# Optimization experiments

Measured on AMD Instinct MI355X. Metric: run time of the kernel, lower is better.

The kernel has to match this reference:

```python
import jax, jax.numpy as jnp
import numpy as np

K = 20
EPS = 1e-6


def _vnt_linear(x, W):
    # VNT linear: rows normalized to sum to 1 (translation-equivariant channel mix)
    Wn = W / W.sum(axis=1, keepdims=True)
    return jnp.einsum('oi,bi...->bo...', Wn, x)


def _vn_lrelu(p, d):
    # Vector-neuron LeakyReLU with negative_slope=0: project p off -d half-space
    dot = jnp.sum(p * d, axis=2, keepdims=True)   # axis 2 is the 3-vector axis
    dns = jnp.sum(d * d, axis=2, keepdims=True)
    return jnp.where(dot >= 0, p, p - (dot / (dns + EPS)) * d)


def _vnt_lin_lrelu(x, W, D):
    p = _vnt_linear(x, W)
    d = jnp.einsum('oi,bi...->bo...', D, x)
    return _vn_lrelu(p, d)


def _graph_feature_cross(pts, k):
    # pts: [B, N, 3] -> edge features [B, 3(ch), 3(vec), N, k]
    B = pts.shape[0]
    xx = jnp.sum(pts * pts, axis=-1)                       # [B, N]
    inner = jnp.einsum('bnd,bmd->bnm', pts, pts)           # [B, N, N]
    pairwise = 2.0 * inner - xx[:, :, None] - xx[:, None, :]  # -||xi-xj||^2
    _, idx = jax.lax.top_k(pairwise, k)                    # [B, N, k]
    b_idx = jnp.arange(B)[:, None, None]
    nbrs = pts[b_idx, idx]                                 # [B, N, k, 3]
    ctr = jnp.broadcast_to(pts[:, :, None, :], nbrs.shape)
    cross = jnp.cross(nbrs, ctr)
    feat = jnp.stack([nbrs - ctr, ctr, cross], axis=3)     # [B, N, k, 3ch, 3vec]
    return jnp.transpose(feat, (0, 3, 4, 1, 2))            # [B, 3, 3, N, k]


def setup_inputs() -> dict:
    key = jax.random.key(0)
    ks = jax.random.split(key, 9)
    B, N, hidden = 8, 2048, 128

    def w(k_, o, i):  # positive weights -> stable row-sum normalization
        return jax.random.uniform(k_, (o, i), jnp.float32, 0.5 / i, 1.5 / i)

    def d(k_, o, i):
        return jax.random.normal(k_, (o, i), jnp.float32) / np.sqrt(i)

    return {
        'pc': jax.random.normal(ks[0], (B, N, 3), jnp.float32),
        'W_pos': w(ks[1], 64, 3), 'D_pos': d(ks[2], 64, 3),
        'W1': w(ks[3], hidden, 64), 'D1': d(ks[4], hidden, 64),
        'W2': w(ks[5], hidden, 2 * hidden), 'D2': d(ks[6], hidden, 2 * hidden),
        'W3': w(ks[7], hidden, 2 * hidden), 'D3': d(ks[8], hidden, 2 * hidden),
    }


def reference(pc, W_pos, D_pos, W1, D1, W2, D2, W3, D3):
    feat = _graph_feature_cross(pc, K)               # [B, 3, 3, N, k]
    net = _vnt_lin_lrelu(feat, W_pos, D_pos)         # [B, 64, 3, N, k]
    net = net.mean(axis=-1)                          # pool over k -> [B, 64, 3, N]
    net = _vnt_lin_lrelu(net, W1, D1)                # [B, 128, 3, N]
    pooled = jnp.broadcast_to(net.mean(axis=-1, keepdims=True), net.shape)
    net = jnp.concatenate([net, pooled], axis=1)     # [B, 256, 3, N]
    net = _vnt_lin_lrelu(net, W2, D2)                # [B, 128, 3, N]
    pooled = jnp.broadcast_to(net.mean(axis=-1, keepdims=True), net.shape)
    net = jnp.concatenate([net, pooled], axis=1)     # [B, 256, 3, N]
    net = _vnt_lin_lrelu(net, W3, D3)                # [B, 128, 3, N]
    c = net.mean(axis=-1)                            # pool over N -> [B, 128, 3]
    return c.reshape(pc.shape[0], -1)                # [B, 384]
```

## Files before the change

### kernel.cpp

```cpp
#include <hip/hip_runtime.h>
#include <hip/hip_bf16.h>
#include <math.h>

constexpr int B = 8;
constexpr int N = 2048;
constexpr int KNN = 20;
constexpr int H = 128;
constexpr int P = 3 * N;
constexpr int QPW = 8;

constexpr int OSB2   = 0;
constexpr int OWT2   = 8448;
constexpr int OWT3   = 41216;
constexpr int OPS1   = 73984;
constexpr int OPS2   = 98560;
constexpr int OOUTS  = 123136;
constexpr int OBAR   = 147712;
constexpr int OSB3   = 148736;
constexpr int OWB1   = 160000;
constexpr int OWB2   = 176384;
constexpr int OWB3   = 209152;
constexpr int OXP0   = 569600;

constexpr int ZERO_BASE = OPS1;
constexpr int ZERO_CNT  = 74752;

constexpr int GRID_VNT  = 1024;
constexpr int BLK_PER_B = 128;

typedef __attribute__((ext_vector_type(8))) short bf16x8;
typedef __attribute__((ext_vector_type(4))) float f32x4;

__device__ __forceinline__ unsigned short f2bf(float x) {
  __hip_bfloat16 h = __float2bfloat16(x);
  return *(unsigned short*)&h;
}
__device__ __forceinline__ float bf2f(unsigned short u) {
  __hip_bfloat16 h;
  *(unsigned short*)&h = u;
  return __bfloat162float(h);
}
__device__ __forceinline__ unsigned int packhl(float x) {
  unsigned short hi = f2bf(x);
  float lo = x - bf2f(hi);
  unsigned short ls = f2bf(lo);
  return (unsigned)hi | ((unsigned)ls << 16);
}

__device__ __forceinline__ float cohload(const float* p) {
  return __hip_atomic_load(p, __ATOMIC_RELAXED, __HIP_MEMORY_SCOPE_AGENT);
}
__device__ __forceinline__ void cohstore(float* p, float v) {
  __hip_atomic_store(p, v, __ATOMIC_RELAXED, __HIP_MEMORY_SCOPE_AGENT);
}

__device__ __forceinline__ void wave_sort_key(unsigned long long& k, int lane) {
#pragma unroll
  for (int kk = 2; kk <= 64; kk <<= 1) {
#pragma unroll
    for (int j = kk >> 1; j > 0; j >>= 1) {
      unsigned long long pk =
          (unsigned long long)__shfl_xor((long long)k, j);
      bool iam_lower   = (lane & j) == 0;
      bool dir_desc    = (lane & kk) == 0;
      bool p_better    = pk > k;
      bool want_better = (dir_desc == iam_lower);
      k = (p_better == want_better) ? pk : k;
    }
  }
}

__global__ __launch_bounds__(512, 8) void knn_edge_kernel(
    const float* __restrict__ pc, const float* __restrict__ Wpos,
    const float* __restrict__ Dp,
    const float* __restrict__ W1, const float* __restrict__ D1,
    const float* __restrict__ W2, const float* __restrict__ D2,
    const float* __restrict__ W3, const float* __restrict__ D3,
    float* __restrict__ ws) {
  __shared__ float4 spt[N];
  __shared__ __align__(16) unsigned char sphase[QPW][640];
  int tid = threadIdx.x;
  int b = blockIdx.y;
  int bid = blockIdx.y * gridDim.x + blockIdx.x;
  int wv = tid >> 6, lane = tid & 63;
  unsigned short* Xp0 = (unsigned short*)(ws + OXP0);
  unsigned short* sbufw = (unsigned short*)sphase[wv];
  float4* erw = (float4*)sphase[wv];

  int o = lane;
  float w0 = Wpos[o * 3 + 0], w1 = Wpos[o * 3 + 1], w2 = Wpos[o * 3 + 2];
  float e0 = Dp[o * 3 + 0], e1 = Dp[o * 3 + 1], e2 = Dp[o * 3 + 2];

  {
    int zi = bid * 512 + tid;
    if (zi < ZERO_CNT) ws[ZERO_BASE + zi] = 0.f;
  }
  if (bid < 96) {
    int rr = bid * 8 + wv;
    const float* src;
    float* tdst = nullptr;
    unsigned int* pdst;
    int C, Cpack;
    bool norm;
    if (rr < 128)      { src = W1 + rr * 64;            C = 64;  Cpack = 64;  norm = true;
                         pdst = (unsigned int*)(ws + OWB1) + rr * 16; }
    else if (rr < 256) { int m = rr - 128; src = D1 + m * 64;  C = 64;  Cpack = 64;  norm = false;
                         pdst = (unsigned int*)(ws + OWB1) + (m + 128) * 16; }
    else if (rr < 384) { int m = rr - 256; src = W2 + m * 256; C = 256; Cpack = 128; norm = true;
                         pdst = (unsigned int*)(ws + OWB2) + m * 16; tdst = ws + OWT2 + m; }
    else if (rr < 512) { int m = rr - 384; src = D2 + m * 256; C = 256; Cpack = 128; norm = false;
                         pdst = (unsigned int*)(ws + OWB2) + (m + 128) * 16; tdst = ws + OWT2 + 128 + m; }
    else if (rr < 640) { int m = rr - 512; src = W3 + m * 256; C = 256; Cpack = 128; norm = true;
                         pdst = (unsigned int*)(ws + OWB3) + m * 16; tdst = ws + OWT3 + m; }
    else               { int m = rr - 640; src = D3 + m * 256; C = 256; Cpack = 128; norm = false;
                         pdst = (unsigned int*)(ws + OWB3) + (m + 128) * 16; tdst = ws + OWT3 + 128 + m; }
    float s = 1.f;
    if (norm) {
      float a = 0.f;
      for (int i = lane; i < C; i += 64) a += src[i];
#pragma unroll
      for (int off = 32; off > 0; off >>= 1) a += __shfl_xor(a, off);
      s = a;
    }
    for (int i = lane; i < C; i += 64) {
      float val = src[i] / s;
      if (i < Cpack) pdst[(i >> 4) * 4096 + (i & 15)] = packhl(val);
      if (tdst && i >= 128) tdst[(i - 128) * 256] = val;
    }
  }

  const float* pcb = pc + (size_t)b * N * 3;
  for (int i = tid; i < N; i += 512) {
    float x = pcb[i * 3 + 0], y = pcb[i * 3 + 1], z = pcb[i * 3 + 2];
    float xx = __fadd_rn(__fadd_rn(__fmul_rn(x, x), __fmul_rn(y, y)), __fmul_rn(z, z));
    spt[i] = make_float4(2.f * x, 2.f * y, 2.f * z, xx);
  }
  __syncthreads();
  int q = blockIdx.x * QPW + wv;
  float4 qp = spt[q];
  float qx = 0.5f * qp.x, qy = 0.5f * qp.y, qz = 0.5f * qp.z, qxx = qp.w;

  float dv[32];
  float lmax = -INFINITY;
#pragma unroll
  for (int i = 0; i < 32; ++i) {
    float4 m = spt[i * 64 + lane];
    float A = __fadd_rn(__fadd_rn(__fmul_rn(m.x, qx), __fmul_rn(m.y, qy)),
                        __fmul_rn(m.z, qz));
    float d = __fsub_rn(__fsub_rn(A, qxx), m.w);
    dv[i] = d;
    lmax = fmaxf(lmax, d);
  }

  float sv = lmax;
#pragma unroll
  for (int k = 2; k <= 64; k <<= 1) {
#pragma unroll
    for (int j = k >> 1; j > 0; j >>= 1) {
      float pv = __shfl_xor(sv, j);
      bool keep_max = ((lane & k) == 0) == ((lane & j) == 0);
      sv = keep_max ? fmaxf(sv, pv) : fminf(sv, pv);
    }
  }
  float tval = __shfl(sv, 19);

  unsigned msk = 0u;
#pragma unroll
  for (int i = 0; i < 32; ++i) msk |= (dv[i] >= tval) ? (1u << i) : 0u;
  int cnt = __popc(msk);
  int scan = cnt;
#pragma unroll
  for (int off = 1; off < 64; off <<= 1) {
    int t = __shfl_up(scan, off);
    scan += (lane >= off) ? t : 0;
  }
  int S = __shfl(scan, 63);
  int pos = scan - cnt;
  unsigned mm = msk;
  while (mm) {
    int i = __ffs(mm) - 1;
    mm &= mm - 1;
    if (pos < 192) sbufw[pos] = (unsigned short)(i * 64 + lane);
    ++pos;
  }

  auto distOf = [&](int m) -> float {
    float4 mp = spt[m];
    float A = __fadd_rn(__fadd_rn(__fmul_rn(mp.x, qx), __fmul_rn(mp.y, qy)),
                        __fmul_rn(mp.z, qz));
    return __fsub_rn(__fsub_rn(A, qxx), mp.w);
  };
  auto mkkey = [&](int m) -> unsigned long long {
    float d = distOf(m);
    unsigned u = __float_as_uint(d);
    u ^= (u >> 31) ? 0xFFFFFFFFu : 0x80000000u;
    return ((unsigned long long)u << 32) | (unsigned)(~m);
  };

  unsigned long long key = 0ULL;
  if (S <= 64) {
    if (lane < S) key = mkkey(sbufw[lane]);
    wave_sort_key(key, lane);
  } else if (S <= 192) {
    int p2 = 0;
    while (p2 < S) {
      if (lane >= KNN) {
        int t = p2 + lane - KNN;
        key = (t < S) ? mkkey(sbufw[t]) : 0ULL;
      }
      wave_sort_key(key, lane);
      p2 += 64 - KNN;
    }
  } else {
    int p2 = 0;
    while (p2 < N) {
      if (lane >= KNN) {
        int t = p2 + lane - KNN;
        key = (t < N) ? mkkey(t) : 0ULL;
      }
      wave_sort_key(key, lane);
      p2 += 64 - KNN;
    }
  }
  int cm = ~((unsigned)key);

  if (lane < KNN) {
    float4 t = spt[cm];
    float nx = 0.5f * t.x, ny = 0.5f * t.y, nz = 0.5f * t.z;
    float ex = nx - qx, ey = ny - qy, ez = nz - qz;
    float rx = ny * qz - nz * qy;
    float ry = nz * qx - nx * qz;
    float rz = nx * qy - ny * qx;
    erw[2 * lane + 0] = make_float4(ex, ey, ez, 0.f);
    erw[2 * lane + 1] = make_float4(rx, ry, rz, 0.f);
  }

  {
    float s = (w0 + w2) + w1;
    w0 = w0 / s; w1 = w1 / s; w2 = w2 / s;
  }
  float cx = qx, cy = qy, cz = qz;
  float pcx = w1 * cx, pcy = w1 * cy, pcz = w1 * cz;
  float dcx = e1 * cx, dcy = e1 * cy, dcz = e1 * cz;
  float ax = 0.f, ay = 0.f, az = 0.f;
#pragma unroll 4
  for (int k = 0; k < KNN; ++k) {
    float4 e4 = erw[2 * k + 0];
    float4 r4 = erw[2 * k + 1];
    float ex = e4.x, ey = e4.y, ez = e4.z;
    float rx = r4.x, ry = r4.y, rz = r4.z;
    float px = fmaf(w0, ex, fmaf(w2, rx, pcx));
    float py = fmaf(w0, ey, fmaf(w2, ry, pcy));
    float pz = fmaf(w0, ez, fmaf(w2, rz, pcz));
    float dx = fmaf(e0, ex, fmaf(e2, rx, dcx));
    float dy = fmaf(e0, ey, fmaf(e2, ry, dcy));
    float dz = fmaf(e0, ez, fmaf(e2, rz, dcz));
    float dot = fmaf(px, dx, fmaf(py, dy, pz * dz));
    float dns = fmaf(dx, dx, fmaf(dy, dy, dz * dz)) + 1e-6f;
    float r0 = __builtin_amdgcn_rcpf(dns);
    r0 = r0 * fmaf(-dns, r0, 2.0f);
    float f = (dot < 0.f) ? dot * r0 : 0.f;
    ax = fmaf(-f, dx, px) + ax;
    ay = fmaf(-f, dy, py) + ay;
    az = fmaf(-f, dz, pz) + az;
  }
  int pbase = ((q >> 4) * 48) + (q & 15);
  unsigned short* dst = Xp0 + ((size_t)b * P + pbase) * 128 + 2 * o;
  *(unsigned int*)(dst)              = packhl(ax * (1.f / 20.f));
  *(unsigned int*)(dst + 16 * 128)   = packhl(ay * (1.f / 20.f));
  *(unsigned int*)(dst + 32 * 128)   = packhl(az * (1.f / 20.f));
}

template <int K2, bool HASPOOL, bool LAST, bool GSRC>
__device__ __forceinline__ void vnt_layer_body(
    unsigned short* xt, float* sb, float* spool,
    const unsigned short* __restrict__ Xp, const unsigned short* __restrict__ Wb,
    const float* __restrict__ ps, const float* __restrict__ Wt,
    float* __restrict__ sbg, unsigned int* sbflag,
    float* __restrict__ pool, float* __restrict__ outs,
    unsigned int* wait_cnt, unsigned int* arrive_cnt,
    int b, int nt, int p0, int tid) {
  constexpr int KS = K2 / 32;
  constexpr int LDR = K2 + 8;
  constexpr int LDO = 132;
  float* ot = (float*)xt;
  int w = tid >> 6, lane = tid & 63;
  int q = lane >> 4, cl = lane & 15;

  if constexpr (GSRC) {
    for (int ch = tid; ch < 48 * (K2 / 8); ch += 256) {
      int rp = ch / (K2 / 8), cc = ch % (K2 / 8);
      *(uint4*)(xt + rp * LDR + cc * 8) =
          *(const uint4*)(Xp + ((size_t)b * P + p0 + rp) * K2 + cc * 8);
    }
  }

  bf16x8 acur[2][2], anxt[2][2];
#pragma unroll
  for (int t = 0; t < 2; ++t)
#pragma unroll
    for (int pd = 0; pd < 2; ++pd)
      acur[t][pd] = *(const bf16x8*)(Wb +
          (size_t)(32 * w + 16 * t + 128 * pd + cl) * 32 + q * 8);

  if constexpr (HASPOOL) {
    if (nt == 0) {
      if (tid == 0) {
        while (__hip_atomic_load(wait_cnt, __ATOMIC_RELAXED,
                                 __HIP_MEMORY_SCOPE_AGENT) < (unsigned)BLK_PER_B) {
          __builtin_amdgcn_s_sleep(2);
        }
      }
      __syncthreads();
      for (int i = tid; i < 384; i += 256) {
        float x = 0.f;
#pragma unroll
        for (int k = 0; k < 8; ++k)
          x += cohload(&ps[k * 3072 + b * 384 + i]);
        spool[i] = x * (1.f / 2048.f);
      }
      __syncthreads();
      float s0 = 0.f, s1 = 0.f, s2 = 0.f;
#pragma unroll 16
      for (int c = 0; c < 128; ++c) {
        float x = Wt[c * 256 + tid];
        s0 = fmaf(x, spool[c * 3 + 0], s0);
        s1 = fmaf(x, spool[c * 3 + 1], s1);
        s2 = fmaf(x, spool[c * 3 + 2], s2);
      }
      sb[tid * 3 + 0] = s0;
      sb[tid * 3 + 1] = s1;
      sb[tid * 3 + 2] = s2;
      cohstore(&sbg[tid * 3 + 0], s0);
      cohstore(&sbg[tid * 3 + 1], s1);
      cohstore(&sbg[tid * 3 + 2], s2);
      __syncthreads();
      if (tid == 0)
        __hip_atomic_fetch_add(sbflag, 1u, __ATOMIC_RELAXED,
                               __HIP_MEMORY_SCOPE_AGENT);
    } else {
      if (tid == 0) {
        while (__hip_atomic_load(sbflag, __ATOMIC_RELAXED,
                                 __HIP_MEMORY_SCOPE_AGENT) < 1u) {
          __builtin_amdgcn_s_sleep(2);
        }
      }
      __syncthreads();
      for (int i = tid; i < 768; i += 256) sb[i] = cohload(&sbg[i]);
      __syncthreads();
    }
  } else {
    __syncthreads();
  }

  f32x4 acc[2][2][3] = {};

#pragma unroll
  for (int ks = 0; ks < KS; ++ks) {
    if (ks + 1 < KS) {
#pragma unroll
      for (int t = 0; t < 2; ++t)
#pragma unroll
        for (int pd = 0; pd < 2; ++pd)
          anxt[t][pd] = *(const bf16x8*)(Wb +
              (size_t)(32 * w + 16 * t + 128 * pd + cl) * 32 + q * 8 +
              (ks + 1) * 8192);
    }
    bf16x8 bb[3];
#pragma unroll
    for (int v = 0; v < 3; ++v)
      bb[v] = *(const bf16x8*)(xt + (v * 16 + cl) * LDR + ks * 32 + q * 8);
#pragma unroll
    for (int t = 0; t < 2; ++t)
#pragma unroll
      for (int pd = 0; pd < 2; ++pd)
#pragma unroll
        for (int v = 0; v < 3; ++v)
          acc[t][pd][v] = __builtin_amdgcn_mfma_f32_16x16x32_bf16(
              acur[t][pd], bb[v], acc[t][pd][v], 0, 0, 0);
#pragma unroll
    for (int t = 0; t < 2; ++t)
#pragma unroll
      for (int pd = 0; pd < 2; ++pd)
        acur[t][pd] = anxt[t][pd];
  }
  __syncthreads();

#pragma unroll
  for (int t = 0; t < 2; ++t) {
    float res[3][4];
#pragma unroll
    for (int r = 0; r < 4; ++r) {
      int o = 32 * w + 16 * t + 4 * q + r;
      float pv[3], dvv[3];
#pragma unroll
      for (int v = 0; v < 3; ++v) {
        pv[v] = acc[t][0][v][r] + (HASPOOL ? sb[o * 3 + v] : 0.f);
        dvv[v] = acc[t][1][v][r] + (HASPOOL ? sb[(128 + o) * 3 + v] : 0.f);
      }
      float dot = fmaf(pv[0], dvv[0], fmaf(pv[1], dvv[1], pv[2] * dvv[2]));
      float dns = fmaf(dvv[0], dvv[0], fmaf(dvv[1], dvv[1], dvv[2] * dvv[2]));
      float f = (dot < 0.f) ? dot / (dns + 1e-6f) : 0.f;
#pragma unroll
      for (int v = 0; v < 3; ++v) res[v][r] = pv[v] - f * dvv[v];
    }
    int o0 = 32 * w + 16 * t + 4 * q;
#pragma unroll
    for (int v = 0; v < 3; ++v) {
      f32x4 rv = {res[v][0], res[v][1], res[v][2], res[v][3]};
      *(f32x4*)(ot + (v * 16 + cl) * LDO + o0) = rv;
    }
  }
  __syncthreads();

  int shadow = (nt & 7) * 3072;
  for (int s = tid; s < 384; s += 256) {
    int o = s / 3, v = s % 3;
    float a2 = 0.f;
#pragma unroll
    for (int c = 0; c < 16; ++c) a2 += ot[(v * 16 + c) * LDO + o];
    if (LAST) atomicAdd(outs + shadow + b * 384 + s, a2);
    else      atomicAdd(pool + shadow + b * 384 + s, a2);
  }

  __syncthreads();
  if (arrive_cnt != nullptr && tid == 0) {
    __hip_atomic_fetch_add(arrive_cnt, 1u, __ATOMIC_RELAXED,
                           __HIP_MEMORY_SCOPE_AGENT);
  }

  if constexpr (!LAST) {
    for (int s = tid; s < 1536; s += 256) {
      int pix = s >> 5, c4 = s & 31;
      float4 sv = *(float4*)(ot + pix * LDO + c4 * 4);
      uint4 vv;
      vv.x = packhl(sv.x);
      vv.y = packhl(sv.y);
      vv.z = packhl(sv.z);
      vv.w = packhl(sv.w);
      *(uint4*)(xt + pix * 264 + c4 * 8) = vv;
    }
  }
}

__global__ __launch_bounds__(256, 4) void vnt_stack_kernel(
    float* __restrict__ ws, float* __restrict__ out) {
  __shared__ __align__(16) char smem[48 * 132 * 4];
  __shared__ float sb[768];
  __shared__ float spool[384];
  __shared__ unsigned int last_flag;
  int tid = threadIdx.x;
  int bid = blockIdx.x;
  int b = bid >> 7;
  int nt = bid & 127;
  int p0 = nt * 48;
  unsigned short* xt = (unsigned short*)smem;
  unsigned int* bar = (unsigned int*)(ws + OBAR);
  unsigned int* cnt1 = bar + b * 32;
  unsigned int* cnt2 = bar + 256 + b * 32;
  unsigned int* cntm = bar + 512;
  unsigned int* sbf2 = bar + 576 + b * 16;
  unsigned int* sbf3 = bar + 704 + b * 16;

  vnt_layer_body<128, false, false, true>(
      xt, sb, spool,
      (const unsigned short*)(ws + OXP0), (const unsigned short*)(ws + OWB1),
      nullptr, nullptr, nullptr, nullptr, ws + OPS1, nullptr,
      nullptr, cnt1, b, nt, p0, tid);

  vnt_layer_body<256, true, false, false>(
      xt, sb, spool,
      nullptr, (const unsigned short*)(ws + OWB2),
      ws + OPS1, ws + OWT2, ws + OSB2 + b * 768, sbf2, ws + OPS2, nullptr,
      cnt1, cnt2, b, nt, p0, tid);

  vnt_layer_body<256, true, true, false>(
      xt, sb, spool,
      nullptr, (const unsigned short*)(ws + OWB3),
      ws + OPS2, ws + OWT3, ws + OSB3 + b * 768, sbf3, nullptr, ws + OOUTS,
      cnt2, nullptr, b, nt, p0, tid);

  if (tid == 0) {
    unsigned old = __hip_atomic_fetch_add(cntm, 1u, __ATOMIC_RELAXED,
                                          __HIP_MEMORY_SCOPE_AGENT);
    last_flag = (old == (unsigned)GRID_VNT - 1) ? 1u : 0u;
  }
  __syncthreads();
  if (last_flag) {
    const float* outs = ws + OOUTS;
    for (int idx = tid; idx < B * 384; idx += 256) {
      float s = 0.f;
#pragma unroll
      for (int k = 0; k < 8; ++k) s += cohload(&outs[k * 3072 + idx]);
      out[idx] = s * (1.f / 2048.f);
    }
  }
}

extern "C" void kernel_launch(void* const* d_in, const int* in_sizes, int n_in,
                              void* d_out, int out_size, void* d_ws, size_t ws_size,
                              hipStream_t stream) {
  (void)in_sizes; (void)n_in; (void)out_size; (void)ws_size;
  const float* pc   = (const float*)d_in[0];
  const float* Wpos = (const float*)d_in[1];
  const float* Dpos = (const float*)d_in[2];
  const float* W1   = (const float*)d_in[3];
  const float* D1   = (const float*)d_in[4];
  const float* W2   = (const float*)d_in[5];
  const float* D2   = (const float*)d_in[6];
  const float* W3   = (const float*)d_in[7];
  const float* D3   = (const float*)d_in[8];
  float* out = (float*)d_out;
  float* ws  = (float*)d_ws;

  knn_edge_kernel<<<dim3(N / QPW, B), 512, 0, stream>>>(
      pc, Wpos, Dpos, W1, D1, W2, D2, W3, D3, ws);

  vnt_stack_kernel<<<GRID_VNT, 256, 0, stream>>>(ws, out);
}
```

Baseline: 164.2 us.

## Fuse kNN edge-feature stage into VNT stack kernel via shared-memory handoff

Result: faster. 157.3 us (median of 2 runs) (-4.2%).

```diff
diff --git a/kernel.cpp b/kernel.cpp
--- a/kernel.cpp
+++ b/kernel.cpp
@@ -7,7 +7,6 @@
 constexpr int KNN = 20;
 constexpr int H = 128;
 constexpr int P = 3 * N;
-constexpr int QPW = 8;
 
 constexpr int OSB2   = 0;
 constexpr int OWT2   = 8448;
@@ -20,10 +19,10 @@
 constexpr int OWB1   = 160000;
 constexpr int OWB2   = 176384;
 constexpr int OWB3   = 209152;
-constexpr int OXP0   = 569600;
 
 constexpr int ZERO_BASE = OPS1;
 constexpr int ZERO_CNT  = 74752;
+constexpr int PREP_BLOCKS = (ZERO_CNT + 255) / 256;
 
 constexpr int GRID_VNT  = 1024;
 constexpr int BLK_PER_B = 128;
@@ -70,211 +69,60 @@
   }
 }
 
-__global__ __launch_bounds__(512, 8) void knn_edge_kernel(
-    const float* __restrict__ pc, const float* __restrict__ Wpos,
-    const float* __restrict__ Dp,
+__global__ __launch_bounds__(256) void prep_kernel(
     const float* __restrict__ W1, const float* __restrict__ D1,
     const float* __restrict__ W2, const float* __restrict__ D2,
     const float* __restrict__ W3, const float* __restrict__ D3,
     float* __restrict__ ws) {
-  __shared__ float4 spt[N];
-  __shared__ __align__(16) unsigned char sphase[QPW][640];
   int tid = threadIdx.x;
-  int b = blockIdx.y;
-  int bid = blockIdx.y * gridDim.x + blockIdx.x;
-  int wv = tid >> 6, lane = tid & 63;
-  unsigned short* Xp0 = (unsigned short*)(ws + OXP0);
-  unsigned short* sbufw = (unsigned short*)sphase[wv];
-  float4* erw = (float4*)sphase[wv];
-
-  int o = lane;
-  float w0 = Wpos[o * 3 + 0], w1 = Wpos[o * 3 + 1], w2 = Wpos[o * 3 + 2];
-  float e0 = Dp[o * 3 + 0], e1 = Dp[o * 3 + 1], e2 = Dp[o * 3 + 2];
-
+  int bid = blockIdx.x;
   {
-    int zi = bid * 512 + tid;
+    int zi = bid * 256 + tid;
     if (zi < ZERO_CNT) ws[ZERO_BASE + zi] = 0.f;
   }
   if (bid < 96) {
-    int rr = bid * 8 + wv;
-    const float* src;
-    float* tdst = nullptr;
-    unsigned int* pdst;
-    int C, Cpack;
-    bool norm;
-    if (rr < 128)      { src = W1 + rr * 64;            C = 64;  Cpack = 64;  norm = true;
-                         pdst = (unsigned int*)(ws + OWB1) + rr * 16; }
-    else if (rr < 256) { int m = rr - 128; src = D1 + m * 64;  C = 64;  Cpack = 64;  norm = false;
-                         pdst = (unsigned int*)(ws + OWB1) + (m + 128) * 16; }
-    else if (rr < 384) { int m = rr - 256; src = W2 + m * 256; C = 256; Cpack = 128; norm = true;
-                         pdst = (unsigned int*)(ws + OWB2) + m * 16; tdst = ws + OWT2 + m; }
-    else if (rr < 512) { int m = rr - 384; src = D2 + m * 256; C = 256; Cpack = 128; norm = false;
-                         pdst = (unsigned int*)(ws + OWB2) + (m + 128) * 16; tdst = ws + OWT2 + 128 + m; }
-    else if (rr < 640) { int m = rr - 512; src = W3 + m * 256; C = 256; Cpack = 128; norm = true;
-                         pdst = (unsigned int*)(ws + OWB3) + m * 16; tdst = ws + OWT3 + m; }
-    else               { int m = rr - 640; src = D3 + m * 256; C = 256; Cpack = 128; norm = false;
-                         pdst = (unsigned int*)(ws + OWB3) + (m + 128) * 16; tdst = ws + OWT3 + 128 + m; }
-    float s = 1.f;
-    if (norm) {
-      float a = 0.f;
-      for (int i = lane; i < C; i += 64) a += src[i];
-#pragma unroll
-      for (int off = 32; off > 0; off >>= 1) a += __shfl_xor(a, off);
-      s = a;
-    }
-    for (int i = lane; i < C; i += 64) {
-      float val = src[i] / s;
-      if (i < Cpack) pdst[(i >> 4) * 4096 + (i & 15)] = packhl(val);
-      if (tdst && i >= 128) tdst[(i - 128) * 256] = val;
-    }
-  }
-
-  const float* pcb = pc + (size_t)b * N * 3;
-  for (int i = tid; i < N; i += 512) {
-    float x = pcb[i * 3 + 0], y = pcb[i * 3 + 1], z = pcb[i * 3 + 2];
-    float xx = __fadd_rn(__fadd_rn(__fmul_rn(x, x), __fmul_rn(y, y)), __fmul_rn(z, z));
-    spt[i] = make_float4(2.f * x, 2.f * y, 2.f * z, xx);
-  }
-  __syncthreads();
-  int q = blockIdx.x * QPW + wv;
-  float4 qp = spt[q];
-  float qx = 0.5f * qp.x, qy = 0.5f * qp.y, qz = 0.5f * qp.z, qxx = qp.w;
-
-  float dv[32];
-  float lmax = -INFINITY;
-#pragma unroll
-  for (int i = 0; i < 32; ++i) {
-    float4 m = spt[i * 64 + lane];
-    float A = __fadd_rn(__fadd_rn(__fmul_rn(m.x, qx), __fmul_rn(m.y, qy)),
-                        __fmul_rn(m.z, qz));
-    float d = __fsub_rn(__fsub_rn(A, qxx), m.w);
-    dv[i] = d;
-    lmax = fmaxf(lmax, d);
-  }
-
-  float sv = lmax;
-#pragma unroll
-  for (int k = 2; k <= 64; k <<= 1) {
-#pragma unroll
-    for (int j = k >> 1; j > 0; j >>= 1) {
-      float pv = __shfl_xor(sv, j);
-      bool keep_max = ((lane & k) == 0) == ((lane & j) == 0);
-      sv = keep_max ? fmaxf(sv, pv) : fminf(sv, pv);
-    }
-  }
-  float tval = __shfl(sv, 19);
-
-  unsigned msk = 0u;
-#pragma unroll
-  for (int i = 0; i < 32; ++i) msk |= (dv[i] >= tval) ? (1u << i) : 0u;
-  int cnt = __popc(msk);
-  int scan = cnt;
-#pragma unroll
-  for (int off = 1; off < 64; off <<= 1) {
-    int t = __shfl_up(scan, off);
-    scan += (lane >= off) ? t : 0;
-  }
-  int S = __shfl(scan, 63);
-  int pos = scan - cnt;
-  unsigned mm = msk;
-  while (mm) {
-    int i = __ffs(mm) - 1;
-    mm &= mm - 1;
-    if (pos < 192) sbufw[pos] = (unsigned short)(i * 64 + lane);
-    ++pos;
-  }
-
-  auto distOf = [&](int m) -> float {
-    float4 mp = spt[m];
-    float A = __fadd_rn(__fadd_rn(__fmul_rn(mp.x, qx), __fmul_rn(mp.y, qy)),
-                        __fmul_rn(mp.z, qz));
-    return __fsub_rn(__fsub_rn(A, qxx), mp.w);
-  };
-  auto mkkey = [&](int m) -> unsigned long long {
-    float d = distOf(m);
-    unsigned u = __float_as_uint(d);
-    u ^= (u >> 31) ? 0xFFFFFFFFu : 0x80000000u;
-    return ((unsigned long long)u << 32) | (unsigned)(~m);
-  };
-
-  unsigned long long key = 0ULL;
-  if (S <= 64) {
-    if (lane < S) key = mkkey(sbufw[lane]);
-    wave_sort_key(key, lane);
-  } else if (S <= 192) {
-    int p2 = 0;
-    while (p2 < S) {
-      if (lane >= KNN) {
-        int t = p2 + lane - KNN;
-        key = (t < S) ? mkkey(sbufw[t]) : 0ULL;
-      }
-      wave_sort_key(key, lane);
-      p2 += 64 - KNN;
-    }
-  } else {
-    int p2 = 0;
-    while (p2 < N) {
-      if (lane >= KNN) {
-        int t = p2 + lane - KNN;
-        key = (t < N) ? mkkey(t) : 0ULL;
-      }
-      wave_sort_key(key, lane);
-      p2 += 64 - KNN;
-    }
-  }
-  int cm = ~((unsigned)key);
-
-  if (lane < KNN) {
-    float4 t = spt[cm];
-    float nx = 0.5f * t.x, ny = 0.5f * t.y, nz = 0.5f * t.z;
-    float ex = nx - qx, ey = ny - qy, ez = nz - qz;
-    float rx = ny * qz - nz * qy;
-    float ry = nz * qx - nx * qz;
-    float rz = nx * qy - ny * qx;
-    erw[2 * lane + 0] = make_float4(ex, ey, ez, 0.f);
-    erw[2 * lane + 1] = make_float4(rx, ry, rz, 0.f);
-  }
-
-  {
-    float s = (w0 + w2) + w1;
-    w0 = w0 / s; w1 = w1 / s; w2 = w2 / s;
-  }
-  float cx = qx, cy = qy, cz = qz;
-  float pcx = w1 * cx, pcy = w1 * cy, pcz = w1 * cz;
-  float dcx = e1 * cx, dcy = e1 * cy, dcz = e1 * cz;
-  float ax = 0.f, ay = 0.f, az = 0.f;
-#pragma unroll 4
-  for (int k = 0; k < KNN; ++k) {
-    float4 e4 = erw[2 * k + 0];
-    float4 r4 = erw[2 * k + 1];
-    float ex = e4.x, ey = e4.y, ez = e4.z;
-    float rx = r4.x, ry = r4.y, rz = r4.z;
-    float px = fmaf(w0, ex, fmaf(w2, rx, pcx));
-    float py = fmaf(w0, ey, fmaf(w2, ry, pcy));
-    float pz = fmaf(w0, ez, fmaf(w2, rz, pcz));
-    float dx = fmaf(e0, ex, fmaf(e2, rx, dcx));
-    float dy = fmaf(e0, ey, fmaf(e2, ry, dcy));
-    float dz = fmaf(e0, ez, fmaf(e2, rz, dcz));
-    float dot = fmaf(px, dx, fmaf(py, dy, pz * dz));
-    float dns = fmaf(dx, dx, fmaf(dy, dy, dz * dz)) + 1e-6f;
-    float r0 = __builtin_amdgcn_rcpf(dns);
-    r0 = r0 * fmaf(-dns, r0, 2.0f);
-    float f = (dot < 0.f) ? dot * r0 : 0.f;
-    ax = fmaf(-f, dx, px) + ax;
-    ay = fmaf(-f, dy, py) + ay;
-    az = fmaf(-f, dz, pz) + az;
-  }
-  int pbase = ((q >> 4) * 48) + (q & 15);
-  unsigned short* dst = Xp0 + ((size_t)b * P + pbase) * 128 + 2 * o;
-  *(unsigned int*)(dst)              = packhl(ax * (1.f / 20.f));
-  *(unsigned int*)(dst + 16 * 128)   = packhl(ay * (1.f / 20.f));
-  *(unsigned int*)(dst + 32 * 128)   = packhl(az * (1.f / 20.f));
-}
-
-template <int K2, bool HASPOOL, bool LAST, bool GSRC>
+    int wv = tid >> 6, lane = tid & 63;
+#pragma unroll
+    for (int r = 0; r < 2; ++r) {
+      int rr = bid * 8 + wv * 2 + r;
+      const float* src;
+      float* tdst = nullptr;
+      unsigned int* pdst;
+      int C, Cpack;
+      bool norm;
+      if (rr < 128)      { src = W1 + rr * 64;            C = 64;  Cpack = 64;  norm = true;
+                           pdst = (unsigned int*)(ws + OWB1) + rr * 16; }
+      else if (rr < 256) { int m = rr - 128; src = D1 + m * 64;  C = 64;  Cpack = 64;  norm = false;
+                           pdst = (unsigned int*)(ws + OWB1) + (m + 128) * 16; }
+      else if (rr < 384) { int m = rr - 256; src = W2 + m * 256; C = 256; Cpack = 128; norm = true;
+                           pdst = (unsigned int*)(ws + OWB2) + m * 16; tdst = ws + OWT2 + m; }
+      else if (rr < 512) { int m = rr - 384; src = D2 + m * 256; C = 256; Cpack = 128; norm = false;
+                           pdst = (unsigned int*)(ws + OWB2) + (m + 128) * 16; tdst = ws + OWT2 + 128 + m; }
+      else if (rr < 640) { int m = rr - 512; src = W3 + m * 256; C = 256; Cpack = 128; norm = true;
+                           pdst = (unsigned int*)(ws + OWB3) + m * 16; tdst = ws + OWT3 + m; }
+      else               { int m = rr - 640; src = D3 + m * 256; C = 256; Cpack = 128; norm = false;
+                           pdst = (unsigned int*)(ws + OWB3) + (m + 128) * 16; tdst = ws + OWT3 + 128 + m; }
+      float s = 1.f;
+      if (norm) {
+        float a = 0.f;
+        for (int i = lane; i < C; i += 64) a += src[i];
+#pragma unroll
+        for (int off = 32; off > 0; off >>= 1) a += __shfl_xor(a, off);
+        s = a;
+      }
+      for (int i = lane; i < C; i += 64) {
+        float val = src[i] / s;
+        if (i < Cpack) pdst[(i >> 4) * 4096 + (i & 15)] = packhl(val);
+        if (tdst && i >= 128) tdst[(i - 128) * 256] = val;
+      }
+    }
+  }
+}
+
+template <int K2, bool HASPOOL, bool LAST>
 __device__ __forceinline__ void vnt_layer_body(
     unsigned short* xt, float* sb, float* spool,
-    const unsigned short* __restrict__ Xp, const unsigned short* __restrict__ Wb,
+    const unsigned short* __restrict__ Wb,
     const float* __restrict__ ps, const float* __restrict__ Wt,
     float* __restrict__ sbg, unsigned int* sbflag,
     float* __restrict__ pool, float* __restrict__ outs,
@@ -286,14 +134,6 @@
   float* ot = (float*)xt;
   int w = tid >> 6, lane = tid & 63;
   int q = lane >> 4, cl = lane & 15;
-
-  if constexpr (GSRC) {
-    for (int ch = tid; ch < 48 * (K2 / 8); ch += 256) {
-      int rp = ch / (K2 / 8), cc = ch % (K2 / 8);
-      *(uint4*)(xt + rp * LDR + cc * 8) =
-          *(const uint4*)(Xp + ((size_t)b * P + p0 + rp) * K2 + cc * 8);
-    }
-  }
 
   bf16x8 acur[2][2], anxt[2][2];
 #pragma unroll
@@ -443,18 +283,26 @@
   }
 }
 
-__global__ __launch_bounds__(256, 4) void vnt_stack_kernel(
-    float* __restrict__ ws, float* __restrict__ out) {
-  __shared__ __align__(16) char smem[48 * 132 * 4];
-  __shared__ float sb[768];
-  __shared__ float spool[384];
+__global__ __launch_bounds__(256, 4) void fused_kernel(
+    const float* __restrict__ pc, const float* __restrict__ Wpos,
+    const float* __restrict__ Dp, float* __restrict__ ws,
+    float* __restrict__ out) {
+  __shared__ __align__(16) char U[35328];
   __shared__ unsigned int last_flag;
-  int tid = threadIdx.x;
+  int tid = threadIdx.x, wv = tid >> 6, lane = tid & 63;
   int bid = blockIdx.x;
   int b = bid >> 7;
   int nt = bid & 127;
   int p0 = nt * 48;
-  unsigned short* xt = (unsigned short*)smem;
+
+  float4* spt = (float4*)U;
+  unsigned char* sph = (unsigned char*)(U + 32768) + wv * 640;
+  unsigned short* sbufw = (unsigned short*)sph;
+  float4* erw = (float4*)sph;
+  unsigned short* xt = (unsigned short*)U;
+  float* sb = (float*)(U + 25344);
+  float* spool = (float*)(U + 28416);
+
   unsigned int* bar = (unsigned int*)(ws + OBAR);
   unsigned int* cnt1 = bar + b * 32;
   unsigned int* cnt2 = bar + 256 + b * 32;
@@ -462,21 +310,178 @@
   unsigned int* sbf2 = bar + 576 + b * 16;
   unsigned int* sbf3 = bar + 704 + b * 16;
 
-  vnt_layer_body<128, false, false, true>(
-      xt, sb, spool,
-      (const unsigned short*)(ws + OXP0), (const unsigned short*)(ws + OWB1),
+  int o = lane;
+  float w0 = Wpos[o * 3 + 0], w1 = Wpos[o * 3 + 1], w2 = Wpos[o * 3 + 2];
+  float e0 = Dp[o * 3 + 0], e1 = Dp[o * 3 + 1], e2 = Dp[o * 3 + 2];
+
+  const float* pcb = pc + (size_t)b * N * 3;
+  for (int i = tid; i < N; i += 256) {
+    float x = pcb[i * 3 + 0], y = pcb[i * 3 + 1], z = pcb[i * 3 + 2];
+    float xx = __fadd_rn(__fadd_rn(__fmul_rn(x, x), __fmul_rn(y, y)), __fmul_rn(z, z));
+    spt[i] = make_float4(2.f * x, 2.f * y, 2.f * z, xx);
+  }
+  __syncthreads();
+
+  {
+    float s = (w0 + w2) + w1;
+    w0 = w0 / s; w1 = w1 / s; w2 = w2 / s;
+  }
+
+  unsigned rx0[4], rx1[4], rx2[4];
+
+#pragma unroll
+  for (int j = 0; j < 4; ++j) {
+    int q = nt * 16 + wv * 4 + j;
+    float4 qp = spt[q];
+    float qx = 0.5f * qp.x, qy = 0.5f * qp.y, qz = 0.5f * qp.z, qxx = qp.w;
+
+    float dv[32];
+    float lmax = -INFINITY;
+#pragma unroll
+    for (int i = 0; i < 32; ++i) {
+      float4 m = spt[i * 64 + lane];
+      float A = __fadd_rn(__fadd_rn(__fmul_rn(m.x, qx), __fmul_rn(m.y, qy)),
+                          __fmul_rn(m.z, qz));
+      float d = __fsub_rn(__fsub_rn(A, qxx), m.w);
+      dv[i] = d;
+      lmax = fmaxf(lmax, d);
+    }
+
+    float sv = lmax;
+#pragma unroll
+    for (int k = 2; k <= 64; k <<= 1) {
+#pragma unroll
+      for (int jj = k >> 1; jj > 0; jj >>= 1) {
+        float pv = __shfl_xor(sv, jj);
+        bool keep_max = ((lane & k) == 0) == ((lane & jj) == 0);
+        sv = keep_max ? fmaxf(sv, pv) : fminf(sv, pv);
+      }
+    }
+    float tval = __shfl(sv, 19);
+
+    unsigned msk = 0u;
+#pragma unroll
+    for (int i = 0; i < 32; ++i) msk |= (dv[i] >= tval) ? (1u << i) : 0u;
+    int cnt = __popc(msk);
+    int scan = cnt;
+#pragma unroll
+    for (int off = 1; off < 64; off <<= 1) {
+      int t = __shfl_up(scan, off);
+      scan += (lane >= off) ? t : 0;
+    }
+    int S = __shfl(scan, 63);
+    int pos = scan - cnt;
+    unsigned mm = msk;
+    while (mm) {
+      int i = __ffs(mm) - 1;
+      mm &= mm - 1;
+      if (pos < 192) sbufw[pos] = (unsigned short)(i * 64 + lane);
+      ++pos;
+    }
+
+    auto distOf = [&](int m) -> float {
+      float4 mp = spt[m];
+      float A = __fadd_rn(__fadd_rn(__fmul_rn(mp.x, qx), __fmul_rn(mp.y, qy)),
+                          __fmul_rn(mp.z, qz));
+      return __fsub_rn(__fsub_rn(A, qxx), mp.w);
+    };
+    auto mkkey = [&](int m) -> unsigned long long {
+      float d = distOf(m);
+      unsigned u = __float_as_uint(d);
+      u ^= (u >> 31) ? 0xFFFFFFFFu : 0x80000000u;
+      return ((unsigned long long)u << 32) | (unsigned)(~m);
+    };
+
+    unsigned long long key = 0ULL;
+    if (S <= 64) {
+      if (lane < S) key = mkkey(sbufw[lane]);
+      wave_sort_key(key, lane);
+    } else if (S <= 192) {
+      int p2 = 0;
+      while (p2 < S) {
+        if (lane >= KNN) {
+          int t = p2 + lane - KNN;
+          key = (t < S) ? mkkey(sbufw[t]) : 0ULL;
+        }
+        wave_sort_key(key, lane);
+        p2 += 64 - KNN;
+      }
+    } else {
+      int p2 = 0;
+      while (p2 < N) {
+        if (lane >= KNN) {
+          int t = p2 + lane - KNN;
+          key = (t < N) ? mkkey(t) : 0ULL;
+        }
+        wave_sort_key(key, lane);
+        p2 += 64 - KNN;
+      }
+    }
+    int cm = ~((unsigned)key);
+
+    if (lane < KNN) {
+      float4 t = spt[cm];
+      float nx = 0.5f * t.x, ny = 0.5f * t.y, nz = 0.5f * t.z;
+      float ex = nx - qx, ey = ny - qy, ez = nz - qz;
+      float rrx = ny * qz - nz * qy;
+      float rry = nz * qx - nx * qz;
+      float rrz = nx * qy - ny * qx;
+      erw[2 * lane + 0] = make_float4(ex, ey, ez, 0.f);
+      erw[2 * lane + 1] = make_float4(rrx, rry, rrz, 0.f);
+    }
+
+    float cx = qx, cy = qy, cz = qz;
+    float pcx = w1 * cx, pcy = w1 * cy, pcz = w1 * cz;
+    float dcx = e1 * cx, dcy = e1 * cy, dcz = e1 * cz;
+    float ax = 0.f, ay = 0.f, az = 0.f;
+#pragma unroll 4
+    for (int k = 0; k < KNN; ++k) {
+      float4 e4 = erw[2 * k + 0];
+      float4 r4 = erw[2 * k + 1];
+      float ex = e4.x, ey = e4.y, ez = e4.z;
+      float rrx = r4.x, rry = r4.y, rrz = r4.z;
+      float px = fmaf(w0, ex, fmaf(w2, rrx, pcx));
+      float py = fmaf(w0, ey, fmaf(w2, rry, pcy));
+      float pz = fmaf(w0, ez, fmaf(w2, rrz, pcz));
+      float dx = fmaf(e0, ex, fmaf(e2, rrx, dcx));
+      float dy = fmaf(e0, ey, fmaf(e2, rry, dcy));
+      float dz = fmaf(e0, ez, fmaf(e2, rrz, dcz));
+      float dot = fmaf(px, dx, fmaf(py, dy, pz * dz));
+      float dns = fmaf(dx, dx, fmaf(dy, dy, dz * dz)) + 1e-6f;
+      float r0 = __builtin_amdgcn_rcpf(dns);
+      r0 = r0 * fmaf(-dns, r0, 2.0f);
+      float f = (dot < 0.f) ? dot * r0 : 0.f;
+      ax = fmaf(-f, dx, px) + ax;
+      ay = fmaf(-f, dy, py) + ay;
+      az = fmaf(-f, dz, pz) + az;
+    }
+    rx0[j] = packhl(ax * (1.f / 20.f));
+    rx1[j] = packhl(ay * (1.f / 20.f));
+    rx2[j] = packhl(az * (1.f / 20.f));
+  }
+
+  __syncthreads();
+
+#pragma unroll
+  for (int j = 0; j < 4; ++j) {
+    int row = wv * 4 + j;
+    *(unsigned int*)(xt + (row + 0)  * 136 + 2 * o) = rx0[j];
+    *(unsigned int*)(xt + (row + 16) * 136 + 2 * o) = rx1[j];
+    *(unsigned int*)(xt + (row + 32) * 136 + 2 * o) = rx2[j];
+  }
+
+  vnt_layer_body<128, false, false>(
+      xt, sb, spool, (const unsigned short*)(ws + OWB1),
       nullptr, nullptr, nullptr, nullptr, ws + OPS1, nullptr,
       nullptr, cnt1, b, nt, p0, tid);
 
-  vnt_layer_body<256, true, false, false>(
-      xt, sb, spool,
-      nullptr, (const unsigned short*)(ws + OWB2),
+  vnt_layer_body<256, true, false>(
+      xt, sb, spool, (const unsigned short*)(ws + OWB2),
       ws + OPS1, ws + OWT2, ws + OSB2 + b * 768, sbf2, ws + OPS2, nullptr,
       cnt1, cnt2, b, nt, p0, tid);
 
-  vnt_layer_body<256, true, true, false>(
-      xt, sb, spool,
-      nullptr, (const unsigned short*)(ws + OWB3),
+  vnt_layer_body<256, true, true>(
+      xt, sb, spool, (const unsigned short*)(ws + OWB3),
       ws + OPS2, ws + OWT3, ws + OSB3 + b * 768, sbf3, nullptr, ws + OOUTS,
       cnt2, nullptr, b, nt, p0, tid);
 
@@ -513,8 +518,7 @@
   float* out = (float*)d_out;
   float* ws  = (float*)d_ws;
 
-  knn_edge_kernel<<<dim3(N / QPW, B), 512, 0, stream>>>(
-      pc, Wpos, Dpos, W1, D1, W2, D2, W3, D3, ws);
-
-  vnt_stack_kernel<<<GRID_VNT, 256, 0, stream>>>(ws, out);
-}
+  prep_kernel<<<PREP_BLOCKS, 256, 0, stream>>>(W1, D1, W2, D2, W3, D3, ws);
+
+  fused_kernel<<<GRID_VNT, 256, 0, stream>>>(pc, Wpos, Dpos, ws, out);
+}
```
